# Performance work log

Hardware: AMD Instinct MI355X
Metric: run time of the kernel (lower is better)

Reference implementation:

```python
import jax, jax.numpy as jnp
import numpy as np

FS = 11        # filter_size
N_ITER = 5     # mean-field iterations


def _unfold(x, fs):
    """x: (B, C, Hp, Wp) padded -> patches (B, C, H, W, fs, fs) with
    patches[b,c,h,w,i,j] == x[b,c,h+i,w+j]."""
    B, C, Hp, Wp = x.shape
    H, W = Hp - fs + 1, Wp - fs + 1
    p = jax.lax.conv_general_dilated_patches(
        x.reshape(B * C, 1, Hp, Wp), (fs, fs), (1, 1), 'VALID')  # (B*C, fs*fs, H, W)
    return p.reshape(B, C, fs, fs, H, W).transpose(0, 1, 4, 5, 2, 3)


def _smoothing_filter(fs, inv_bw, spacings):
    """Gaussian spatial filter with zeroed center, shape (B, fs, fs)."""
    r = jnp.arange(-(fs // 2), fs // 2 + 1, dtype=spacings.dtype)
    d = jnp.stack(jnp.meshgrid(r, r, indexing='ij'))           # (2, fs, fs)
    d = d[None] * spacings[:, :, None, None]                   # (B, 2, fs, fs)
    f = jnp.exp(-jnp.sum((d * inv_bw) ** 2 / 2, axis=1))       # (B, fs, fs)
    return f.at[:, fs // 2, fs // 2].set(0.0)


def setup_inputs() -> dict:
    key = jax.random.key(0)
    k1, k2 = jax.random.split(key)
    B, C, CH, H, W = 2, 6, 3, 192, 192
    return {
        'x': jax.random.normal(k1, (B, C, H, W), dtype=jnp.float32),
        'features': jax.random.normal(k2, (B, CH, H, W), dtype=jnp.float32),
        'spatial_spacings': jnp.ones((B, 2), dtype=jnp.float32),
        'smoothing_weight': jnp.array(1.0, dtype=jnp.float32),
        'appearance_weight': jnp.array(1.0, dtype=jnp.float32),
        'inverse_smoothing_bandwidth': jnp.array(1.0, dtype=jnp.float32),
        'inverse_appearance_bandwidth': jnp.array(1.0, dtype=jnp.float32),
    }


def reference(x, features, spatial_spacings, smoothing_weight, appearance_weight,
              inverse_smoothing_bandwidth, inverse_appearance_bandwidth):
    fs, pad = FS, FS // 2
    B, C, H, W = x.shape
    pad_cfg = [(0, 0), (0, 0), (pad, pad), (pad, pad)]

    # Spatial Gaussian filter (iteration-independent).
    sf = _smoothing_filter(fs, inverse_smoothing_bandwidth, spatial_spacings)  # (B,fs,fs)

    # Bilateral (appearance) filter, also iteration-independent -> hoisted.
    fpatch = _unfold(jnp.pad(features, pad_cfg), fs)           # (B,ch,H,W,fs,fs)
    diffs = features[..., None, None] - fpatch
    af = jnp.exp(-jnp.sum((diffs * inverse_appearance_bandwidth) ** 2 / 2, axis=1))  # (B,H,W,fs,fs)
    af = af.at[..., fs // 2, fs // 2].set(0.0)

    # combined message filter: w_s * sf + w_a * sf * af  (center tap already zero)
    sfb = sf[:, None, None]                                    # (B,1,1,fs,fs)
    total_filter = smoothing_weight * jnp.broadcast_to(sfb, af.shape) + appearance_weight * sfb * af

    compat = -jnp.eye(C, dtype=x.dtype)                        # Potts compatibility mu(l,l') = -[l==l']
    negative_unary = x
    for _ in range(N_ITER):
        q = jax.nn.softmax(x, axis=1)
        qpatch = _unfold(jnp.pad(q, pad_cfg), fs)              # (B,C,H,W,fs,fs)
        msg = jnp.einsum('bhwij,bchwij->bchw', total_filter, qpatch)
        x = negative_unary - jnp.einsum('bjhw,jk->bkhw', msg, compat)
    return jax.nn.log_softmax(x, axis=1)
```

## Files before the change

kernel.cpp:

```cpp
#include <hip/hip_runtime.h>

#define HH 192
#define WW 192
#define BB 2
#define NC 6
#define FSZ 11
#define PAD 5
#define TW 16
#define TH 8
#define SWD 26
#define SHT 18
#define LA 33
#define HW (HH*WW)
#define BT 512

__device__ __forceinline__ unsigned pkbf(float a, float b) {
    unsigned ua = (__float_as_uint(a) + 0x8000u) >> 16;
    unsigned ub = (__float_as_uint(b) + 0x8000u) & 0xffff0000u;
    return ua | ub;
}
__device__ __forceinline__ float lo16(unsigned u){ return __uint_as_float(u << 16); }
__device__ __forceinline__ float hi16(unsigned u){ return __uint_as_float(u & 0xffff0000u); }

template<bool FIRST, bool LAST>
__global__ __launch_bounds__(BT, 4)
void crf_iter(const float* __restrict__ xpl, const uint4* __restrict__ Ain,
              const float* __restrict__ f2in, const float* __restrict__ feats,
              const float* __restrict__ spac, const float* __restrict__ swp,
              const float* __restrict__ awp, const float* __restrict__ isbp,
              const float* __restrict__ iabp,
              uint4* __restrict__ Aout, float* __restrict__ f2out,
              float* __restrict__ outp)
{
    __shared__ uint4 A[SHT][LA];
    __shared__ float F2[SHT][LA];
    __shared__ float sfw[FSZ*FSZ];
    __shared__ float sfa[FSZ*FSZ];
    __shared__ float pm[8][NC][132];

    const int tid = threadIdx.x;
    const int b  = blockIdx.z;
    const int w0 = blockIdx.x * TW;
    const int h0 = blockIdx.y * TH;

    const float swv = swp[0], awv = awp[0], isb = isbp[0], iab = iabp[0];
    const float s0 = spac[b*2], s1 = spac[b*2+1];
    const float sfac = iab * 0.70710678f;

    if (tid < FSZ*FSZ) {
        const int fi = tid / FSZ, fj = tid - (tid/FSZ)*FSZ;
        const float ri = (float)(fi-PAD) * s0 * isb;
        const float rj = (float)(fj-PAD) * s1 * isb;
        float sf = __expf(-0.5f*(ri*ri + rj*rj));
        if (fi == PAD && fj == PAD) sf = 0.f;
        sfw[tid] = sf * swv;
        sfa[tid] = sf * awv;
    }

    for (int idx = tid; idx < SHT*SWD; idx += BT) {
        const int sr = idx / SWD, sc = idx - (idx/SWD)*SWD;
        const int gh = h0 + sr - PAD, gw = w0 + sc - PAD;
        uint4 av = make_uint4(0u,0u,0u,0u);
        float f2v = 0.f;
        if (gh >= 0 && gh < HH && gw >= 0 && gw < WW) {
            if (FIRST) {
                const int off = gh*WW + gw;
                const float* xb = xpl + (size_t)b*NC*HW + off;
                const float v0 = xb[0];
                const float v1 = xb[HW];
                const float v2 = xb[2*HW];
                const float v3 = xb[3*HW];
                const float v4 = xb[4*HW];
                const float v5 = xb[5*HW];
                float m = fmaxf(fmaxf(fmaxf(v0,v1),fmaxf(v2,v3)),fmaxf(v4,v5));
                float q0=__expf(v0-m), q1=__expf(v1-m), q2=__expf(v2-m);
                float q3=__expf(v3-m), q4=__expf(v4-m), q5=__expf(v5-m);
                const float rs = 1.0f/(q0+q1+q2+q3+q4+q5);
                q0*=rs; q1*=rs; q2*=rs; q3*=rs; q4*=rs; q5*=rs;
                const float* fb = feats + (size_t)b*3*HW + off;
                const float g0 = fb[0]*sfac, g1 = fb[HW]*sfac, g2 = fb[2*HW]*sfac;
                av = make_uint4(pkbf(q0,q1), pkbf(q2,q3), pkbf(q4,q5), pkbf(g0,g1));
                f2v = g2;
            } else {
                const size_t p = (size_t)(b*HH + gh)*WW + gw;
                av  = Ain[p];
                f2v = f2in[p];
            }
        }
        A[sr][sc]  = av;
        F2[sr][sc] = f2v;
    }

    const int w    = tid >> 6;
    const int l    = tid & 63;
    const int half = l >> 5;
    const int lh   = l & 31;
    const int ry   = lh >> 2;
    const int lc0  = (lh & 3) * 4;
    const int jb   = half * 6;

    __syncthreads();

    float cf0[4], cf1[4], cf2[4];
    #pragma unroll
    for (int k = 0; k < 4; ++k) {
        const unsigned fw = A[ry+PAD][lc0+PAD+k].w;
        cf0[k] = lo16(fw);
        cf1[k] = hi16(fw);
        cf2[k] = F2[ry+PAD][lc0+PAD+k];
    }

    float msg[4][NC];
    #pragma unroll
    for (int k = 0; k < 4; ++k)
        #pragma unroll
        for (int c = 0; c < NC; ++c) msg[k][c] = 0.f;

    auto row_pass = [&](int i) {
        const int r = ry + i;
        const uint4* Ar = &A[r][lc0 + jb];
        const float* Fr = &F2[r][lc0 + jb];
        float srwR[6], sraR[6];
        #pragma unroll
        for (int d = 0; d < 6; ++d) {
            const int jj = jb + d;
            const bool v = (jj < FSZ);
            srwR[d] = v ? sfw[i*FSZ + jj] : 0.f;
            sraR[d] = v ? sfa[i*FSZ + jj] : 0.f;
        }
        #pragma unroll
        for (int a = 0; a < 8; ++a) {
            const uint4 av = Ar[a];
            const float g2 = Fr[a];
            const float q0 = lo16(av.x), q1 = hi16(av.x);
            const float q2 = lo16(av.y), q3 = hi16(av.y);
            const float q4 = lo16(av.z), q5 = hi16(av.z);
            const float g0 = lo16(av.w), g1 = hi16(av.w);
            #pragma unroll
            for (int k = 0; k < 4; ++k) {
                const int d = a - k;
                if (d < 0 || d > 5) continue;
                const float d0 = cf0[k]-g0, d1 = cf1[k]-g1, d2 = cf2[k]-g2;
                const float t  = fmaf(d2,d2, fmaf(d1,d1, d0*d0));
                const float af = __expf(-t);
                const float tf = fmaf(af, sraR[d], srwR[d]);
                msg[k][0] = fmaf(tf,q0,msg[k][0]);
                msg[k][1] = fmaf(tf,q1,msg[k][1]);
                msg[k][2] = fmaf(tf,q2,msg[k][2]);
                msg[k][3] = fmaf(tf,q3,msg[k][3]);
                msg[k][4] = fmaf(tf,q4,msg[k][4]);
                msg[k][5] = fmaf(tf,q5,msg[k][5]);
            }
        }
        if (jb == 0) {
            const uint4 av = Ar[8];
            const float g2 = Fr[8];
            const float q0 = lo16(av.x), q1 = hi16(av.x);
            const float q2 = lo16(av.y), q3 = hi16(av.y);
            const float q4 = lo16(av.z), q5 = hi16(av.z);
            const float g0 = lo16(av.w), g1 = hi16(av.w);
            const float d0 = cf0[3]-g0, d1 = cf1[3]-g1, d2 = cf2[3]-g2;
            const float t  = fmaf(d2,d2, fmaf(d1,d1, d0*d0));
            const float af = __expf(-t);
            const float tf = fmaf(af, sraR[5], srwR[5]);
            msg[3][0] = fmaf(tf,q0,msg[3][0]);
            msg[3][1] = fmaf(tf,q1,msg[3][1]);
            msg[3][2] = fmaf(tf,q2,msg[3][2]);
            msg[3][3] = fmaf(tf,q3,msg[3][3]);
            msg[3][4] = fmaf(tf,q4,msg[3][4]);
            msg[3][5] = fmaf(tf,q5,msg[3][5]);
        }
    };

    row_pass(w);
    if (w < 3) row_pass(w + 8);

    #pragma unroll
    for (int k = 0; k < 4; ++k)
        #pragma unroll
        for (int c = 0; c < NC; ++c)
            msg[k][c] += __shfl_xor(msg[k][c], 32);

    if (half == 0) {
        #pragma unroll
        for (int c = 0; c < NC; ++c) {
            float4 v = make_float4(msg[0][c], msg[1][c], msg[2][c], msg[3][c]);
            *(float4*)&pm[w][c][ry*16 + lc0] = v;
        }
    }
    __syncthreads();

    if (tid < TW*TH) {
        const int col = tid & 15, rw = tid >> 4;
        float xn[NC];
        #pragma unroll
        for (int c = 0; c < NC; ++c) {
            float s = 0.f;
            #pragma unroll
            for (int g = 0; g < 8; ++g) s += pm[g][c][tid];
            xn[c] = s;
        }
        const int gh = h0 + rw, gw = w0 + col;
        const size_t pb = (size_t)b*NC*HW + (size_t)gh*WW + gw;
        #pragma unroll
        for (int c = 0; c < NC; ++c) xn[c] += xpl[pb + (size_t)c*HW];

        float m = xn[0];
        #pragma unroll
        for (int c = 1; c < NC; ++c) m = fmaxf(m, xn[c]);

        if (LAST) {
            float s = 0.f;
            #pragma unroll
            for (int c = 0; c < NC; ++c) s += __expf(xn[c]-m);
            const float lg = m + __logf(s);
            #pragma unroll
            for (int c = 0; c < NC; ++c) outp[pb + (size_t)c*HW] = xn[c] - lg;
        } else {
            float e[NC]; float s = 0.f;
            #pragma unroll
            for (int c = 0; c < NC; ++c) { e[c] = __expf(xn[c]-m); s += e[c]; }
            const float rs = 1.0f / s;
            const unsigned f01 = A[rw+PAD][col+PAD].w;
            const size_t p = (size_t)(b*HH + gh)*WW + gw;
            Aout[p] = make_uint4(pkbf(e[0]*rs, e[1]*rs),
                                 pkbf(e[2]*rs, e[3]*rs),
                                 pkbf(e[4]*rs, e[5]*rs), f01);
            if (FIRST) f2out[p] = F2[rw+PAD][col+PAD];
        }
    }
}

extern "C" void kernel_launch(void* const* d_in, const int* in_sizes, int n_in,
                              void* d_out, int out_size, void* d_ws, size_t ws_size,
                              hipStream_t stream)
{
    const float* x    = (const float*)d_in[0];
    const float* fts  = (const float*)d_in[1];
    const float* spc  = (const float*)d_in[2];
    const float* swp  = (const float*)d_in[3];
    const float* awp  = (const float*)d_in[4];
    const float* isbp = (const float*)d_in[5];
    const float* iabp = (const float*)d_in[6];
    float* out = (float*)d_out;

    uint4* A0  = (uint4*)d_ws;
    uint4* A1  = A0 + (size_t)BB*HW;
    float* f2s = (float*)(A1 + (size_t)BB*HW);

    dim3 grid(WW/TW, HH/TH, BB);
    dim3 blk(BT);

    crf_iter<true ,false><<<grid, blk, 0, stream>>>(x, A1, f2s, fts, spc, swp, awp, isbp, iabp, A0, f2s, out);
    crf_iter<false,false><<<grid, blk, 0, stream>>>(x, A0, f2s, fts, spc, swp, awp, isbp, iabp, A1, f2s, out);
    crf_iter<false,false><<<grid, blk, 0, stream>>>(x, A1, f2s, fts, spc, swp, awp, isbp, iabp, A0, f2s, out);
    crf_iter<false,false><<<grid, blk, 0, stream>>>(x, A0, f2s, fts, spc, swp, awp, isbp, iabp, A1, f2s, out);
    crf_iter<false,true ><<<grid, blk, 0, stream>>>(x, A1, f2s, fts, spc, swp, awp, isbp, iabp, A0, f2s, out);
}
```

Measured before the change: 64.34 us.

## Rebalance filter rows across twelve waves to remove uneven per-wave work

Raises the block from 8 to 12 wavefronts and splits the 11 filter rows so each wave handles one row segment. The middle row is divided between two waves instead of three waves doing two rows each. This is meant to remove the load imbalance where some waves did double work, and it shrinks the shared-memory row pitch. In exchange it adds more partial-sum buffers to reduce and uses a larger block with a different occupancy target.

```diff
diff --git a/kernel.cpp b/kernel.cpp
--- a/kernel.cpp
+++ b/kernel.cpp
@@ -10,9 +10,11 @@
 #define TH 8
 #define SWD 26
 #define SHT 18
-#define LA 33
+#define LA 27
 #define HW (HH*WW)
-#define BT 512
+#define NWV 12
+#define BT (NWV*64)
+#define NPX (TW*TH)
 
 __device__ __forceinline__ unsigned pkbf(float a, float b) {
     unsigned ua = (__float_as_uint(a) + 0x8000u) >> 16;
@@ -23,28 +25,28 @@
 __device__ __forceinline__ float hi16(unsigned u){ return __uint_as_float(u & 0xffff0000u); }
 
 template<bool FIRST, bool LAST>
-__global__ __launch_bounds__(BT, 4)
-void crf_iter(const float* __restrict__ xpl, const uint4* __restrict__ Ain,
-              const float* __restrict__ f2in, const float* __restrict__ feats,
-              const float* __restrict__ spac, const float* __restrict__ swp,
-              const float* __restrict__ awp, const float* __restrict__ isbp,
-              const float* __restrict__ iabp,
-              uint4* __restrict__ Aout, float* __restrict__ f2out,
-              float* __restrict__ outp)
+__global__ __launch_bounds__(BT, 6)
+void crf_it(const float* __restrict__ xpl, const uint4* __restrict__ Ain,
+            const float* __restrict__ f2in, const float* __restrict__ feats,
+            const float* __restrict__ spac, const float* __restrict__ swp,
+            const float* __restrict__ awp, const float* __restrict__ isbp,
+            const float* __restrict__ iabp,
+            uint4* __restrict__ Aout, float* __restrict__ f2out,
+            float* __restrict__ outp)
 {
     __shared__ uint4 A[SHT][LA];
     __shared__ float F2[SHT][LA];
     __shared__ float sfw[FSZ*FSZ];
     __shared__ float sfa[FSZ*FSZ];
-    __shared__ float pm[8][NC][132];
+    __shared__ float pm[NWV][NC][132];
 
     const int tid = threadIdx.x;
     const int b  = blockIdx.z;
     const int w0 = blockIdx.x * TW;
     const int h0 = blockIdx.y * TH;
 
-    const float swv = swp[0], awv = awp[0], isb = isbp[0], iab = iabp[0];
-    const float s0 = spac[b*2], s1 = spac[b*2+1];
+    const float sw  = swp[0], aw = awp[0], isb = isbp[0], iab = iabp[0];
+    const float s0  = spac[b*2], s1 = spac[b*2+1];
     const float sfac = iab * 0.70710678f;
 
     if (tid < FSZ*FSZ) {
@@ -53,12 +55,12 @@
         const float rj = (float)(fj-PAD) * s1 * isb;
         float sf = __expf(-0.5f*(ri*ri + rj*rj));
         if (fi == PAD && fj == PAD) sf = 0.f;
-        sfw[tid] = sf * swv;
-        sfa[tid] = sf * awv;
-    }
-
-    for (int idx = tid; idx < SHT*SWD; idx += BT) {
-        const int sr = idx / SWD, sc = idx - (idx/SWD)*SWD;
+        sfw[tid] = sf * sw;
+        sfa[tid] = sf * aw;
+    }
+
+    if (tid < SHT*SWD) {
+        const int sr = tid / SWD, sc = tid - (tid/SWD)*SWD;
         const int gh = h0 + sr - PAD, gw = w0 + sc - PAD;
         uint4 av = make_uint4(0u,0u,0u,0u);
         float f2v = 0.f;
@@ -66,21 +68,17 @@
             if (FIRST) {
                 const int off = gh*WW + gw;
                 const float* xb = xpl + (size_t)b*NC*HW + off;
-                const float v0 = xb[0];
-                const float v1 = xb[HW];
-                const float v2 = xb[2*HW];
-                const float v3 = xb[3*HW];
-                const float v4 = xb[4*HW];
-                const float v5 = xb[5*HW];
+                const float v0 = xb[0], v1 = xb[HW], v2 = xb[2*HW];
+                const float v3 = xb[3*HW], v4 = xb[4*HW], v5 = xb[5*HW];
                 float m = fmaxf(fmaxf(fmaxf(v0,v1),fmaxf(v2,v3)),fmaxf(v4,v5));
                 float q0=__expf(v0-m), q1=__expf(v1-m), q2=__expf(v2-m);
                 float q3=__expf(v3-m), q4=__expf(v4-m), q5=__expf(v5-m);
                 const float rs = 1.0f/(q0+q1+q2+q3+q4+q5);
-                q0*=rs; q1*=rs; q2*=rs; q3*=rs; q4*=rs; q5*=rs;
                 const float* fb = feats + (size_t)b*3*HW + off;
-                const float g0 = fb[0]*sfac, g1 = fb[HW]*sfac, g2 = fb[2*HW]*sfac;
-                av = make_uint4(pkbf(q0,q1), pkbf(q2,q3), pkbf(q4,q5), pkbf(g0,g1));
-                f2v = g2;
+                const float g0 = fb[0]*sfac, g1 = fb[HW]*sfac;
+                f2v = fb[2*HW]*sfac;
+                av = make_uint4(pkbf(q0*rs,q1*rs), pkbf(q2*rs,q3*rs),
+                                pkbf(q4*rs,q5*rs), pkbf(g0,g1));
             } else {
                 const size_t p = (size_t)(b*HH + gh)*WW + gw;
                 av  = Ain[p];
@@ -90,46 +88,50 @@
         A[sr][sc]  = av;
         F2[sr][sc] = f2v;
     }
+    __syncthreads();
 
     const int w    = tid >> 6;
     const int l    = tid & 63;
     const int half = l >> 5;
     const int lh   = l & 31;
     const int ry   = lh >> 2;
-    const int lc0  = (lh & 3) * 4;
-    const int jb   = half * 6;
-
-    __syncthreads();
+    const int c0   = (lh & 3) * 4;
+
+    int row, jbase, jcnt;
+    if (w == 5)       { row = 5; jbase = half ? 6 : 0; jcnt = 3; }
+    else if (w == 11) { row = 5; jbase = half ? 9 : 3; jcnt = half ? 2 : 3; }
+    else              { row = w; jbase = half ? 6 : 0; jcnt = half ? 5 : 6; }
+    const int asteps = jcnt + 3;
+
+    float srwR[6], sraR[6];
+    #pragma unroll
+    for (int d = 0; d < 6; ++d) {
+        const int j = jbase + d;
+        const bool v = (d < jcnt) && (j < FSZ);
+        srwR[d] = v ? sfw[row*FSZ + j] : 0.f;
+        sraR[d] = v ? sfa[row*FSZ + j] : 0.f;
+    }
 
     float cf0[4], cf1[4], cf2[4];
     #pragma unroll
     for (int k = 0; k < 4; ++k) {
-        const unsigned fw = A[ry+PAD][lc0+PAD+k].w;
+        const unsigned fw = A[ry+PAD][c0+PAD+k].w;
         cf0[k] = lo16(fw);
         cf1[k] = hi16(fw);
-        cf2[k] = F2[ry+PAD][lc0+PAD+k];
-    }
-
-    float msg[4][NC];
-    #pragma unroll
-    for (int k = 0; k < 4; ++k)
-        #pragma unroll
-        for (int c = 0; c < NC; ++c) msg[k][c] = 0.f;
-
-    auto row_pass = [&](int i) {
-        const int r = ry + i;
-        const uint4* Ar = &A[r][lc0 + jb];
-        const float* Fr = &F2[r][lc0 + jb];
-        float srwR[6], sraR[6];
-        #pragma unroll
-        for (int d = 0; d < 6; ++d) {
-            const int jj = jb + d;
-            const bool v = (jj < FSZ);
-            srwR[d] = v ? sfw[i*FSZ + jj] : 0.f;
-            sraR[d] = v ? sfa[i*FSZ + jj] : 0.f;
-        }
-        #pragma unroll
-        for (int a = 0; a < 8; ++a) {
+        cf2[k] = F2[ry+PAD][c0+PAD+k];
+    }
+
+    float2 m01[4], m23[4], m45[4];
+    #pragma unroll
+    for (int k = 0; k < 4; ++k) {
+        m01[k]=make_float2(0.f,0.f); m23[k]=make_float2(0.f,0.f); m45[k]=make_float2(0.f,0.f);
+    }
+
+    const uint4* Ar = &A[ry + row][c0 + jbase];
+    const float* Fr = &F2[ry + row][c0 + jbase];
+    #pragma unroll
+    for (int a = 0; a < 9; ++a) {
+        if (a < asteps) {
             const uint4 av = Ar[a];
             const float g2 = Fr[a];
             const float q0 = lo16(av.x), q1 = hi16(av.x);
@@ -139,71 +141,49 @@
             #pragma unroll
             for (int k = 0; k < 4; ++k) {
                 const int d = a - k;
-                if (d < 0 || d > 5) continue;
-                const float d0 = cf0[k]-g0, d1 = cf1[k]-g1, d2 = cf2[k]-g2;
-                const float t  = fmaf(d2,d2, fmaf(d1,d1, d0*d0));
-                const float af = __expf(-t);
-                const float tf = fmaf(af, sraR[d], srwR[d]);
-                msg[k][0] = fmaf(tf,q0,msg[k][0]);
-                msg[k][1] = fmaf(tf,q1,msg[k][1]);
-                msg[k][2] = fmaf(tf,q2,msg[k][2]);
-                msg[k][3] = fmaf(tf,q3,msg[k][3]);
-                msg[k][4] = fmaf(tf,q4,msg[k][4]);
-                msg[k][5] = fmaf(tf,q5,msg[k][5]);
+                if (0 <= d && d < 6) {
+                    const float d0 = cf0[k]-g0, d1 = cf1[k]-g1, d2 = cf2[k]-g2;
+                    const float t  = fmaf(d2,d2, fmaf(d1,d1, d0*d0));
+                    const float af = __expf(-t);
+                    const float tf = fmaf(af, sraR[d], srwR[d]);
+                    m01[k].x = fmaf(tf,q0,m01[k].x); m01[k].y = fmaf(tf,q1,m01[k].y);
+                    m23[k].x = fmaf(tf,q2,m23[k].x); m23[k].y = fmaf(tf,q3,m23[k].y);
+                    m45[k].x = fmaf(tf,q4,m45[k].x); m45[k].y = fmaf(tf,q5,m45[k].y);
+                }
             }
         }
-        if (jb == 0) {
-            const uint4 av = Ar[8];
-            const float g2 = Fr[8];
-            const float q0 = lo16(av.x), q1 = hi16(av.x);
-            const float q2 = lo16(av.y), q3 = hi16(av.y);
-            const float q4 = lo16(av.z), q5 = hi16(av.z);
-            const float g0 = lo16(av.w), g1 = hi16(av.w);
-            const float d0 = cf0[3]-g0, d1 = cf1[3]-g1, d2 = cf2[3]-g2;
-            const float t  = fmaf(d2,d2, fmaf(d1,d1, d0*d0));
-            const float af = __expf(-t);
-            const float tf = fmaf(af, sraR[5], srwR[5]);
-            msg[3][0] = fmaf(tf,q0,msg[3][0]);
-            msg[3][1] = fmaf(tf,q1,msg[3][1]);
-            msg[3][2] = fmaf(tf,q2,msg[3][2]);
-            msg[3][3] = fmaf(tf,q3,msg[3][3]);
-            msg[3][4] = fmaf(tf,q4,msg[3][4]);
-            msg[3][5] = fmaf(tf,q5,msg[3][5]);
-        }
-    };
-
-    row_pass(w);
-    if (w < 3) row_pass(w + 8);
-
-    #pragma unroll
-    for (int k = 0; k < 4; ++k)
-        #pragma unroll
-        for (int c = 0; c < NC; ++c)
-            msg[k][c] += __shfl_xor(msg[k][c], 32);
+    }
+
+    #pragma unroll
+    for (int k = 0; k < 4; ++k) {
+        m01[k].x += __shfl_xor(m01[k].x, 32); m01[k].y += __shfl_xor(m01[k].y, 32);
+        m23[k].x += __shfl_xor(m23[k].x, 32); m23[k].y += __shfl_xor(m23[k].y, 32);
+        m45[k].x += __shfl_xor(m45[k].x, 32); m45[k].y += __shfl_xor(m45[k].y, 32);
+    }
 
     if (half == 0) {
-        #pragma unroll
-        for (int c = 0; c < NC; ++c) {
-            float4 v = make_float4(msg[0][c], msg[1][c], msg[2][c], msg[3][c]);
-            *(float4*)&pm[w][c][ry*16 + lc0] = v;
-        }
+        const int px = ry*16 + c0;
+        *(float4*)&pm[w][0][px] = make_float4(m01[0].x, m01[1].x, m01[2].x, m01[3].x);
+        *(float4*)&pm[w][1][px] = make_float4(m01[0].y, m01[1].y, m01[2].y, m01[3].y);
+        *(float4*)&pm[w][2][px] = make_float4(m23[0].x, m23[1].x, m23[2].x, m23[3].x);
+        *(float4*)&pm[w][3][px] = make_float4(m23[0].y, m23[1].y, m23[2].y, m23[3].y);
+        *(float4*)&pm[w][4][px] = make_float4(m45[0].x, m45[1].x, m45[2].x, m45[3].x);
+        *(float4*)&pm[w][5][px] = make_float4(m45[0].y, m45[1].y, m45[2].y, m45[3].y);
     }
     __syncthreads();
 
-    if (tid < TW*TH) {
-        const int col = tid & 15, rw = tid >> 4;
+    if (tid < NPX) {
+        const int pr = tid >> 4, pc = tid & 15;
+        const int oh = h0 + pr, ow = w0 + pc;
+        const size_t pb = (size_t)b*NC*HW + (size_t)oh*WW + ow;
         float xn[NC];
         #pragma unroll
         for (int c = 0; c < NC; ++c) {
             float s = 0.f;
             #pragma unroll
-            for (int g = 0; g < 8; ++g) s += pm[g][c][tid];
-            xn[c] = s;
-        }
-        const int gh = h0 + rw, gw = w0 + col;
-        const size_t pb = (size_t)b*NC*HW + (size_t)gh*WW + gw;
-        #pragma unroll
-        for (int c = 0; c < NC; ++c) xn[c] += xpl[pb + (size_t)c*HW];
+            for (int g = 0; g < NWV; ++g) s += pm[g][c][tid];
+            xn[c] = s + xpl[pb + (size_t)c*HW];
+        }
 
         float m = xn[0];
         #pragma unroll
@@ -217,16 +197,15 @@
             #pragma unroll
             for (int c = 0; c < NC; ++c) outp[pb + (size_t)c*HW] = xn[c] - lg;
         } else {
-            float e[NC]; float s = 0.f;
+            float e[NC], s = 0.f;
             #pragma unroll
             for (int c = 0; c < NC; ++c) { e[c] = __expf(xn[c]-m); s += e[c]; }
             const float rs = 1.0f / s;
-            const unsigned f01 = A[rw+PAD][col+PAD].w;
-            const size_t p = (size_t)(b*HH + gh)*WW + gw;
-            Aout[p] = make_uint4(pkbf(e[0]*rs, e[1]*rs),
-                                 pkbf(e[2]*rs, e[3]*rs),
-                                 pkbf(e[4]*rs, e[5]*rs), f01);
-            if (FIRST) f2out[p] = F2[rw+PAD][col+PAD];
+            const int r5 = pr + PAD, c5 = pc + PAD;
+            const size_t p = (size_t)(b*HH + oh)*WW + ow;
+            Aout[p] = make_uint4(pkbf(e[0]*rs,e[1]*rs), pkbf(e[2]*rs,e[3]*rs),
+                                 pkbf(e[4]*rs,e[5]*rs), A[r5][c5].w);
+            if (FIRST) f2out[p] = F2[r5][c5];
         }
     }
 }
@@ -251,9 +230,9 @@
     dim3 grid(WW/TW, HH/TH, BB);
     dim3 blk(BT);
 
-    crf_iter<true ,false><<<grid, blk, 0, stream>>>(x, A1, f2s, fts, spc, swp, awp, isbp, iabp, A0, f2s, out);
-    crf_iter<false,false><<<grid, blk, 0, stream>>>(x, A0, f2s, fts, spc, swp, awp, isbp, iabp, A1, f2s, out);
-    crf_iter<false,false><<<grid, blk, 0, stream>>>(x, A1, f2s, fts, spc, swp, awp, isbp, iabp, A0, f2s, out);
-    crf_iter<false,false><<<grid, blk, 0, stream>>>(x, A0, f2s, fts, spc, swp, awp, isbp, iabp, A1, f2s, out);
-    crf_iter<false,true ><<<grid, blk, 0, stream>>>(x, A1, f2s, fts, spc, swp, awp, isbp, iabp, A0, f2s, out);
+    crf_it<true ,false><<<grid, blk, 0, stream>>>(x, A1, f2s, fts, spc, swp, awp, isbp, iabp, A0, f2s, out);
+    crf_it<false,false><<<grid, blk, 0, stream>>>(x, A0, f2s, fts, spc, swp, awp, isbp, iabp, A1, f2s, out);
+    crf_it<false,false><<<grid, blk, 0, stream>>>(x, A1, f2s, fts, spc, swp, awp, isbp, iabp, A0, f2s, out);
+    crf_it<false,false><<<grid, blk, 0, stream>>>(x, A0, f2s, fts, spc, swp, awp, isbp, iabp, A1, f2s, out);
+    crf_it<false,true ><<<grid, blk, 0, stream>>>(x, A1, f2s, fts, spc, swp, awp, isbp, iabp, A0, f2s, out);
 }
```

After: 63.01 us. -2.1%, faster.
